# Performance work log

Measured on AMD Instinct MI355X. Metric: run time of the kernel, lower is better.

## Reference

```python
import jax, jax.numpy as jnp
import numpy as np

B = 16384
D = 768           # roberta hidden
SENT = 3          # sentiment features
GRU_IN = D + SENT # 771
H = 128           # memory_dim
FUSION = GRU_IN + H + D  # 1667
E = 7             # num_emotions
S = 65536         # number of (dialog, speaker) memory slots


def setup_inputs() -> dict:
    key = jax.random.key(0)
    ks = jax.random.split(key, 12)
    inp = {
        "h_t": jax.random.normal(ks[0], (B, D), jnp.float32),
        "h_ctx": jax.random.normal(ks[1], (B, D), jnp.float32),
        "sentiment": jax.random.uniform(ks[2], (B, SENT), jnp.float32),
        "slot_ids": jax.random.randint(ks[3], (B,), 0, S, jnp.int32),
        # speaker memory table (gathered/scattered by slot_ids)
        "memory": jax.random.normal(ks[4], (S, H), jnp.float32) * 0.1,
        # GRUCell params (torch layout: rows ordered [r; z; n])
        "W_ih": jax.random.normal(ks[5], (3 * H, GRU_IN), jnp.float32) * 0.02,
        "W_hh": jax.random.normal(ks[6], (3 * H, H), jnp.float32) * 0.02,
        "b_ih": jnp.zeros((3 * H,), jnp.float32),
        "b_hh": jnp.zeros((3 * H,), jnp.float32),
        # heads
        "W_e": jax.random.normal(ks[7], (E, FUSION), jnp.float32) * 0.02,
        "b_e": jnp.zeros((E,), jnp.float32),
        "W_s": jax.random.normal(ks[8], (1, FUSION), jnp.float32) * 0.02,
        "b_s": jnp.zeros((1,), jnp.float32),
    }
    return inp


def _gru_cell(x, h, W_ih, W_hh, b_ih, b_hh):
    # x: [B, GRU_IN], h: [B, H]; torch nn.GRUCell semantics
    gi = x @ W_ih.T + b_ih            # [B, 3H]
    gh = h @ W_hh.T + b_hh            # [B, 3H]
    i_r, i_z, i_n = jnp.split(gi, 3, axis=1)
    h_r, h_z, h_n = jnp.split(gh, 3, axis=1)
    r = jax.nn.sigmoid(i_r + h_r)
    z = jax.nn.sigmoid(i_z + h_z)
    n = jnp.tanh(i_n + r * h_n)
    return (1.0 - z) * n + z * h


def reference(h_t, h_ctx, sentiment, slot_ids, memory, W_ih, W_hh, b_ih, b_hh, W_e, b_e, W_s, b_s):
    h_t_aug = jnp.concatenate([h_t, sentiment], axis=1)      # [B, 771]
    s_t = memory[slot_ids]                                    # gather  [B, H]
    s_new = _gru_cell(h_t_aug, s_t, W_ih, W_hh, b_ih, b_hh)   # [B, H]
    # prediction uses the PRE-update memory s_t (as in the torch loop)
    z_t = jnp.concatenate([h_t_aug, s_t, h_ctx], axis=1)      # [B, 1667] (dropout is identity in eval)
    emotion_logits = z_t @ W_e.T + b_e                        # [B, E]
    shift_logits = (z_t @ W_s.T + b_s)[:, 0]                  # [B]
    # matching the sequential dict updates in the original loop)
    new_memory = memory.at[slot_ids].set(s_new)               # [S, H]
    return emotion_logits, shift_logits, new_memory
```

## Files before the change

kernel.cpp:

```cpp
#include <hip/hip_runtime.h>
#include <hip/hip_bf16.h>

#define B_SZ   16384
#define D_SZ   768
#define H_SZ   128
#define S_SZ   65536
#define E_SZ   7

#define NFR    33
#define NSTEP  53

typedef __attribute__((ext_vector_type(8))) short bf16x8;
typedef __attribute__((ext_vector_type(4))) float f32x4;
typedef __attribute__((ext_vector_type(4))) unsigned int u32x4;

#define LD4(p) (*reinterpret_cast<const float4*>(p))
#define MFMA(d, a, b) d = __builtin_amdgcn_mfma_f32_16x16x32_bf16(a, b, d, 0, 0, 0)

#define GLDS(gp, lp) __builtin_amdgcn_global_load_lds(                              \
        (const __attribute__((address_space(1))) unsigned int*)(gp),                \
        (__attribute__((address_space(3))) unsigned int*)(lp), 16, 0, 0)
#define GLDSN(gp, lp) __builtin_amdgcn_global_load_lds(                             \
        (const __attribute__((address_space(1))) unsigned int*)(gp),                \
        (__attribute__((address_space(3))) unsigned int*)(lp), 16, 0, 2)

#define PIPE_BAR(N) do {                                                            \
        asm volatile("s_waitcnt vmcnt(" #N ")" ::: "memory");                       \
        __builtin_amdgcn_sched_barrier(0);                                          \
        __builtin_amdgcn_s_barrier();                                               \
    } while (0)

static __device__ __forceinline__ ushort f2bf(float v) {
    unsigned u = __float_as_uint(v);
    u = (u + 0x7FFFu + ((u >> 16) & 1u)) >> 16;
    return (ushort)u;
}

static __device__ __forceinline__ unsigned pk2(float x, float y) {
    unsigned a = __float_as_uint(x) + 0x8000u;
    unsigned b = __float_as_uint(y) + 0x8000u;
    return __builtin_amdgcn_perm(b, a, 0x07060302);
}

static __device__ __forceinline__ bf16x8 cvt8(float4 a, float4 b) {
    union { unsigned u[4]; bf16x8 v; } r;
    r.u[0] = pk2(a.x, a.y); r.u[1] = pk2(a.z, a.w);
    r.u[2] = pk2(b.x, b.y); r.u[3] = pk2(b.z, b.w);
    return r.v;
}

static __device__ __forceinline__ float w2_value(int n, int k,
    const float* __restrict__ W_ih, const float* __restrict__ W_hh,
    const float* __restrict__ b_ih, const float* __restrict__ b_hh,
    const float* __restrict__ W_e,  const float* __restrict__ b_e,
    const float* __restrict__ W_s,  const float* __restrict__ b_s)
{
    float v = 0.0f;
    if (n < 256) {
        if (k < 768)                        v = W_ih[(size_t)n * 771 + k];
        else if (k < 896)                   v = W_hh[(size_t)n * 128 + (k - 768)];
        else if (k >= 1664 && k < 1667)     v = W_ih[(size_t)n * 771 + 768 + (k - 1664)];
        else if (k == 1667)                 v = b_ih[n] + b_hh[n];
    } else if (n < 384) {
        if (k < 768)                        v = W_ih[(size_t)n * 771 + k];
        else if (k >= 1664 && k < 1667)     v = W_ih[(size_t)n * 771 + 768 + (k - 1664)];
        else if (k == 1667)                 v = b_ih[n];
    } else if (n < 512) {
        int g = n - 128;
        if (k >= 768 && k < 896)            v = W_hh[(size_t)g * 128 + (k - 768)];
        else if (k == 1667)                 v = b_hh[g];
    } else if (n < 520) {
        int e = n - 512;
        const float* Wr = (e < E_SZ) ? (W_e + (size_t)e * 1667) : W_s;
        if (k < 768)                        v = Wr[k];
        else if (k < 896)                   v = Wr[771 + (k - 768)];
        else if (k < 1664)                  v = Wr[899 + (k - 896)];
        else if (k < 1667)                  v = Wr[768 + (k - 1664)];
        else if (k == 1667)                 v = (e < E_SZ) ? b_e[e] : b_s[0];
    }
    return v;
}

__global__ __launch_bounds__(256) void pack_w2f_kernel(
    const float* __restrict__ W_ih, const float* __restrict__ W_hh,
    const float* __restrict__ b_ih, const float* __restrict__ b_hh,
    const float* __restrict__ W_e,  const float* __restrict__ b_e,
    const float* __restrict__ W_s,  const float* __restrict__ b_s,
    ushort* __restrict__ W2f)
{
    int tid = blockIdx.x * 256 + threadIdx.x;
    if (tid >= NFR * NSTEP * 64) return;
    int lane  = tid & 63;
    int kstep = (tid >> 6) % NSTEP;
    int nf    = tid / (NSTEP * 64);
    int n     = nf * 16 + (lane & 15);
    int kbase = kstep * 32 + (lane >> 4) * 8;
    ushort o[8];
#pragma unroll
    for (int j = 0; j < 8; ++j)
        o[j] = f2bf(w2_value(n, kbase + j, W_ih, W_hh, b_ih, b_hh, W_e, b_e, W_s, b_s));
    *reinterpret_cast<uint4*>(W2f + (size_t)tid * 8) = *reinterpret_cast<const uint4*>(o);
}

__global__ __launch_bounds__(256) void winner_kernel(const int* __restrict__ slot_ids,
                                                     int* __restrict__ winner)
{
    int b = blockIdx.x * 256 + threadIdx.x;
    if (b < B_SZ) atomicMax(&winner[slot_ids[b]], b);
}

static __device__ __forceinline__ bf16x8 ldB(const ushort* __restrict__ W2f, int nf, int ks, int lane) {
    return *reinterpret_cast<const bf16x8*>(W2f + ((size_t)(nf * NSTEP + ks) * 64 + lane) * 8);
}

static __device__ __forceinline__ float4 lds_rd(const char* Ab, int st, int row, int h) {
    return *reinterpret_cast<const float4*>(Ab + st * 4096 + row * 128 + ((h ^ (row & 7)) << 4));
}

__global__ __launch_bounds__(512, 4) void fused_kernel(
    const float* __restrict__ h_t,   const float* __restrict__ h_ctx,
    const float* __restrict__ sent,  const int* __restrict__ slot_ids,
    const float* __restrict__ memory,const ushort* __restrict__ W2f,
    const int* __restrict__ winner,
    float* __restrict__ out_emo, float* __restrict__ out_shift, float* __restrict__ out_mem)
{
    __shared__ alignas(16) char  A_st[3 * 16384];
    __shared__ alignas(16) f32x4 redh[2][8 * 64];

    const int tid  = threadIdx.x;
    const int wave = tid >> 6;
    const int lane = tid & 63;
    const int row0 = blockIdx.x * 32;
    const int cl   = lane & 15, kg = lane >> 4;

    const int fR = wave, fZ = 8 + wave, fI = 16 + wave, fH = 24 + wave;

    const int sst   = wave >> 2;
    const int srb   = wave & 3;
    const int srow  = srb * 8 + (lane >> 3);
    const int scg   = (lane & 7) ^ (srow & 7);
    const int sslot = slot_ids[row0 + srow];

    f32x4 z4 = {0.f, 0.f, 0.f, 0.f};
    f32x4 aR0 = z4, aZ0 = z4, aI0 = z4, aH0 = z4;
    f32x4 aR1 = z4, aZ1 = z4, aI1 = z4, aH1 = z4;
    f32x4 hc0 = z4, hc1 = z4;

#define STAGE(C, BASE) do { _Pragma("unroll")                                             \
    for (int q = 0; q < 2; ++q) {                                                         \
        const int st_ = sst + 2 * q;                                                      \
        const int s_  = 4 * (C) + st_;                                                    \
        char* dst_ = (BASE) + st_ * 4096 + srb * 1024;                                    \
        if (s_ < 24)      GLDSN(h_t + (size_t)(row0 + srow) * D_SZ + s_ * 32 + scg * 4, dst_);          \
        else if (s_ < 28) GLDS(memory + (size_t)sslot * H_SZ + (s_ - 24) * 32 + scg * 4, dst_);         \
        else              GLDSN(h_ctx + (size_t)(row0 + srow) * D_SZ + (s_ - 28) * 32 + scg * 4, dst_); \
    } } while (0)

    STAGE(0, A_st); STAGE(1, A_st + 16384);
    PIPE_BAR(2);

    int bc = 0, sb = 2;

#pragma unroll 1
    for (int c = 0; c < 6; ++c) {
        const char* Ab = A_st + bc * 16384;
#pragma unroll
        for (int st = 0; st < 4; ++st) {
            const int s = c * 4 + st;
            bf16x8 B0 = ldB(W2f, fR, s, lane), B1 = ldB(W2f, fZ, s, lane), B2 = ldB(W2f, fI, s, lane);
            float4 x0 = lds_rd(Ab, st, cl, 2 * kg), x1 = lds_rd(Ab, st, cl, 2 * kg + 1);
            bf16x8 a0 = cvt8(x0, x1);
            MFMA(aR0, a0, B0); MFMA(aZ0, a0, B1); MFMA(aI0, a0, B2);
            float4 y0 = lds_rd(Ab, st, 16 + cl, 2 * kg), y1 = lds_rd(Ab, st, 16 + cl, 2 * kg + 1);
            bf16x8 a1 = cvt8(y0, y1);
            MFMA(aR1, a1, B0); MFMA(aZ1, a1, B1); MFMA(aI1, a1, B2);
            if ((s & 7) == wave) {
                bf16x8 Bh = ldB(W2f, 32, s, lane);
                MFMA(hc0, a0, Bh); MFMA(hc1, a1, Bh);
            }
        }
        STAGE(c + 2, A_st + sb * 16384);
        PIPE_BAR(2);
        bc = (bc == 2) ? 0 : bc + 1;
        sb = (sb == 2) ? 0 : sb + 1;
    }

    {
        const char* Ab = A_st + bc * 16384;
#pragma unroll
        for (int t = 0; t < 4; ++t) {
            const int s = 24 + t;
            bf16x8 B0 = ldB(W2f, fR, s, lane), B1 = ldB(W2f, fZ, s, lane), B2 = ldB(W2f, fH, s, lane);
            float4 x0 = lds_rd(Ab, t, cl, 2 * kg), x1 = lds_rd(Ab, t, cl, 2 * kg + 1);
            bf16x8 a0 = cvt8(x0, x1);
            MFMA(aR0, a0, B0); MFMA(aZ0, a0, B1); MFMA(aH0, a0, B2);
            float4 y0 = lds_rd(Ab, t, 16 + cl, 2 * kg), y1 = lds_rd(Ab, t, 16 + cl, 2 * kg + 1);
            bf16x8 a1 = cvt8(y0, y1);
            MFMA(aR1, a1, B0); MFMA(aZ1, a1, B1); MFMA(aH1, a1, B2);
            if (t == wave) {
                bf16x8 Bh = ldB(W2f, 32, s, lane);
                MFMA(hc0, a0, Bh); MFMA(hc1, a1, Bh);
            }
        }
        STAGE(8, A_st + sb * 16384);
        PIPE_BAR(2);
        bc = (bc == 2) ? 0 : bc + 1;
        sb = (sb == 2) ? 0 : sb + 1;
    }

#pragma unroll 1
    for (int c = 7; c <= 10; ++c) {
        const char* Ab = A_st + bc * 16384;
        if ((c & 1) == (wave >> 2)) {
            const int st = wave & 3;
            const int s  = c * 4 + st;
            bf16x8 Bh = ldB(W2f, 32, s, lane);
            float4 x0 = lds_rd(Ab, st, cl, 2 * kg), x1 = lds_rd(Ab, st, cl, 2 * kg + 1);
            MFMA(hc0, cvt8(x0, x1), Bh);
            float4 y0 = lds_rd(Ab, st, 16 + cl, 2 * kg), y1 = lds_rd(Ab, st, 16 + cl, 2 * kg + 1);
            MFMA(hc1, cvt8(y0, y1), Bh);
        }
        STAGE(c + 2, A_st + sb * 16384);
        PIPE_BAR(2);
        bc = (bc == 2) ? 0 : bc + 1;
        sb = (sb == 2) ? 0 : sb + 1;
    }

    {
        const char* Ab = A_st + bc * 16384;
        if ((wave >> 2) == 1) {
            const int st = wave & 3;
            bf16x8 Bh = ldB(W2f, 32, 44 + st, lane);
            float4 x0 = lds_rd(Ab, st, cl, 2 * kg), x1 = lds_rd(Ab, st, cl, 2 * kg + 1);
            MFMA(hc0, cvt8(x0, x1), Bh);
            float4 y0 = lds_rd(Ab, st, 16 + cl, 2 * kg), y1 = lds_rd(Ab, st, 16 + cl, 2 * kg + 1);
            MFMA(hc1, cvt8(y0, y1), Bh);
        }
        PIPE_BAR(0);
        bc = (bc == 2) ? 0 : bc + 1;
    }

    {
        const char* Ab = A_st + bc * 16384;
        if ((wave >> 2) == 0) {
            const int st = wave & 3;
            bf16x8 Bh = ldB(W2f, 32, 48 + st, lane);
            float4 x0 = lds_rd(Ab, st, cl, 2 * kg), x1 = lds_rd(Ab, st, cl, 2 * kg + 1);
            MFMA(hc0, cvt8(x0, x1), Bh);
            float4 y0 = lds_rd(Ab, st, 16 + cl, 2 * kg), y1 = lds_rd(Ab, st, 16 + cl, 2 * kg + 1);
            MFMA(hc1, cvt8(y0, y1), Bh);
        }
        const int rA0 = row0 + cl, rA1 = rA0 + 16;
        bf16x8 a0, a1;
#pragma unroll
        for (int jj = 0; jj < 8; ++jj) {
            int kk = kg * 8 + jj;
            float v0 = 0.f, v1 = 0.f;
            if (kk < 3)       { v0 = sent[(size_t)rA0 * 3 + kk]; v1 = sent[(size_t)rA1 * 3 + kk]; }
            else if (kk == 3) { v0 = 1.f; v1 = 1.f; }
            a0[jj] = (short)f2bf(v0); a1[jj] = (short)f2bf(v1);
        }
        bf16x8 T0 = ldB(W2f, fR, 52, lane), T1 = ldB(W2f, fZ, 52, lane);
        bf16x8 T2 = ldB(W2f, fI, 52, lane), T3 = ldB(W2f, fH, 52, lane);
        MFMA(aR0, a0, T0); MFMA(aZ0, a0, T1); MFMA(aI0, a0, T2); MFMA(aH0, a0, T3);
        MFMA(aR1, a1, T0); MFMA(aZ1, a1, T1); MFMA(aI1, a1, T2); MFMA(aH1, a1, T3);
        if (wave == 4) {
            bf16x8 Bh = ldB(W2f, 32, 52, lane);
            MFMA(hc0, a0, Bh); MFMA(hc1, a1, Bh);
        }
        const int j = 16 * wave + cl;
#pragma unroll
        for (int rg = 0; rg < 2; ++rg) {
            const f32x4 rv = rg ? aR1 : aR0, zv = rg ? aZ1 : aZ0;
            const f32x4 iv = rg ? aI1 : aI0, hv4 = rg ? aH1 : aH0;
#pragma unroll
            for (int rr = 0; rr < 4; ++rr) {
                const int row  = row0 + rg * 16 + kg * 4 + rr;
                const int slot = slot_ids[row];
                const bool win = (winner[slot] == row);
                float rgate = 1.0f / (1.0f + __expf(-rv[rr]));
                float zg    = 1.0f / (1.0f + __expf(-zv[rr]));
                float nn    = tanhf(iv[rr] + rgate * hv4[rr]);
                float h     = memory[(size_t)slot * H_SZ + j];
                float sn    = (1.0f - zg) * nn + zg * h;
                if (win) out_mem[(size_t)slot * H_SZ + j] = sn;
            }
        }
    }

#pragma unroll 1
    for (int k = 0; k < 8; ++k) {
        int idx  = k * 512 + tid;
        int rr   = idx >> 5;
        int c4   = (idx & 31) * 4;
        int slot = blockIdx.x * 128 + rr;
        if (winner[slot] < 0) {
            u32x4 v = __builtin_nontemporal_load(
                reinterpret_cast<const u32x4*>(memory + (size_t)slot * H_SZ + c4));
            __builtin_nontemporal_store(v,
                reinterpret_cast<u32x4*>(out_mem + (size_t)slot * H_SZ + c4));
        }
    }

    __syncthreads();
    redh[0][wave * 64 + lane] = hc0;
    redh[1][wave * 64 + lane] = hc1;
    __syncthreads();
    if (tid < 128) {
        const int rg = tid >> 6, l = tid & 63;
        f32x4 hv = redh[rg][l];
#pragma unroll
        for (int w = 1; w < 8; ++w) hv += redh[rg][w * 64 + l];
        const int col  = l & 15;
        const int rowb = row0 + rg * 16 + (l >> 4) * 4;
#pragma unroll
        for (int rr = 0; rr < 4; ++rr) {
            const int row = rowb + rr;
            if (col < E_SZ)       out_emo[(size_t)row * E_SZ + col] = hv[rr];
            else if (col == E_SZ) out_shift[row] = hv[rr];
        }
    }
#undef STAGE
}

extern "C" void kernel_launch(void* const* d_in, const int* in_sizes, int n_in,
                              void* d_out, int out_size, void* d_ws, size_t ws_size,
                              hipStream_t stream)
{
    const float* h_t     = (const float*)d_in[0];
    const float* h_ctx   = (const float*)d_in[1];
    const float* sent    = (const float*)d_in[2];
    const int*   slot_ids= (const int*)  d_in[3];
    const float* memory  = (const float*)d_in[4];
    const float* W_ih    = (const float*)d_in[5];
    const float* W_hh    = (const float*)d_in[6];
    const float* b_ih    = (const float*)d_in[7];
    const float* b_hh    = (const float*)d_in[8];
    const float* W_e     = (const float*)d_in[9];
    const float* b_e     = (const float*)d_in[10];
    const float* W_s     = (const float*)d_in[11];
    const float* b_s     = (const float*)d_in[12];

    float* out       = (float*)d_out;
    float* out_emo   = out;
    float* out_shift = out + (size_t)B_SZ * E_SZ;
    float* out_mem   = out + (size_t)B_SZ * E_SZ + B_SZ;

    int*    winner = (int*)d_ws;
    ushort* W2f    = (ushort*)((char*)d_ws + (size_t)S_SZ * sizeof(int));

    hipMemsetAsync(winner, 0xFF, (size_t)S_SZ * sizeof(int), stream);

    pack_w2f_kernel<<<(NFR * NSTEP * 64 + 255) / 256, 256, 0, stream>>>(
        W_ih, W_hh, b_ih, b_hh, W_e, b_e, W_s, b_s, W2f);
    winner_kernel<<<B_SZ / 256, 256, 0, stream>>>(slot_ids, winner);
    fused_kernel<<<B_SZ / 32, 512, 0, stream>>>(
        h_t, h_ctx, sent, slot_ids, memory, W2f, winner, out_emo, out_shift, out_mem);
}
```

Before: 74.46 us.

## Halve LDS staging chunk size and reduction buffer to double occupancy

Shrinks each pipeline stage from four k-steps to two, cutting the triple-buffered LDS staging area from 48KB to 24KB. The head reduction now reuses a single buffer across two passes. Launch bounds go from 4 to 8 blocks per CU so more blocks can be resident to hide gather and load latency. The cost is twice as many pipeline barriers and stage iterations, plus a tighter register budget per thread that may cause spills.

Result: slower. 130.8 us (+75.7%).

```diff
diff --git a/kernel.cpp b/kernel.cpp
--- a/kernel.cpp
+++ b/kernel.cpp
@@ -117,15 +117,15 @@
     return *reinterpret_cast<const float4*>(Ab + st * 4096 + row * 128 + ((h ^ (row & 7)) << 4));
 }
 
-__global__ __launch_bounds__(512, 4) void fused_kernel(
+__global__ __launch_bounds__(512, 8) void fused_kernel(
     const float* __restrict__ h_t,   const float* __restrict__ h_ctx,
     const float* __restrict__ sent,  const int* __restrict__ slot_ids,
     const float* __restrict__ memory,const ushort* __restrict__ W2f,
     const int* __restrict__ winner,
     float* __restrict__ out_emo, float* __restrict__ out_shift, float* __restrict__ out_mem)
 {
-    __shared__ alignas(16) char  A_st[3 * 16384];
-    __shared__ alignas(16) f32x4 redh[2][8 * 64];
+    __shared__ alignas(16) char  A_st[3 * 8192];
+    __shared__ alignas(16) f32x4 redh[8 * 64];
 
     const int tid  = threadIdx.x;
     const int wave = tid >> 6;
@@ -146,27 +146,25 @@
     f32x4 aR1 = z4, aZ1 = z4, aI1 = z4, aH1 = z4;
     f32x4 hc0 = z4, hc1 = z4;
 
-#define STAGE(C, BASE) do { _Pragma("unroll")                                             \
-    for (int q = 0; q < 2; ++q) {                                                         \
-        const int st_ = sst + 2 * q;                                                      \
-        const int s_  = 4 * (C) + st_;                                                    \
-        char* dst_ = (BASE) + st_ * 4096 + srb * 1024;                                    \
+#define STAGE(C, BASE) do {                                                               \
+        const int s_ = 2 * (C) + sst;                                                     \
+        char* dst_ = (BASE) + sst * 4096 + srb * 1024;                                    \
         if (s_ < 24)      GLDSN(h_t + (size_t)(row0 + srow) * D_SZ + s_ * 32 + scg * 4, dst_);          \
         else if (s_ < 28) GLDS(memory + (size_t)sslot * H_SZ + (s_ - 24) * 32 + scg * 4, dst_);         \
         else              GLDSN(h_ctx + (size_t)(row0 + srow) * D_SZ + (s_ - 28) * 32 + scg * 4, dst_); \
-    } } while (0)
-
-    STAGE(0, A_st); STAGE(1, A_st + 16384);
-    PIPE_BAR(2);
+    } while (0)
+
+    STAGE(0, A_st); STAGE(1, A_st + 8192);
+    PIPE_BAR(1);
 
     int bc = 0, sb = 2;
 
 #pragma unroll 1
-    for (int c = 0; c < 6; ++c) {
-        const char* Ab = A_st + bc * 16384;
-#pragma unroll
-        for (int st = 0; st < 4; ++st) {
-            const int s = c * 4 + st;
+    for (int c = 0; c < 12; ++c) {
+        const char* Ab = A_st + bc * 8192;
+#pragma unroll
+        for (int st = 0; st < 2; ++st) {
+            const int s = c * 2 + st;
             bf16x8 B0 = ldB(W2f, fR, s, lane), B1 = ldB(W2f, fZ, s, lane), B2 = ldB(W2f, fI, s, lane);
             float4 x0 = lds_rd(Ab, st, cl, 2 * kg), x1 = lds_rd(Ab, st, cl, 2 * kg + 1);
             bf16x8 a0 = cvt8(x0, x1);
@@ -179,76 +177,85 @@
                 MFMA(hc0, a0, Bh); MFMA(hc1, a1, Bh);
             }
         }
-        STAGE(c + 2, A_st + sb * 16384);
-        PIPE_BAR(2);
+        STAGE(c + 2, A_st + sb * 8192);
+        PIPE_BAR(1);
         bc = (bc == 2) ? 0 : bc + 1;
         sb = (sb == 2) ? 0 : sb + 1;
     }
 
-    {
-        const char* Ab = A_st + bc * 16384;
-#pragma unroll
-        for (int t = 0; t < 4; ++t) {
-            const int s = 24 + t;
+#pragma unroll 1
+    for (int c = 12; c < 14; ++c) {
+        const char* Ab = A_st + bc * 8192;
+#pragma unroll
+        for (int st = 0; st < 2; ++st) {
+            const int s = c * 2 + st;
             bf16x8 B0 = ldB(W2f, fR, s, lane), B1 = ldB(W2f, fZ, s, lane), B2 = ldB(W2f, fH, s, lane);
-            float4 x0 = lds_rd(Ab, t, cl, 2 * kg), x1 = lds_rd(Ab, t, cl, 2 * kg + 1);
+            float4 x0 = lds_rd(Ab, st, cl, 2 * kg), x1 = lds_rd(Ab, st, cl, 2 * kg + 1);
             bf16x8 a0 = cvt8(x0, x1);
             MFMA(aR0, a0, B0); MFMA(aZ0, a0, B1); MFMA(aH0, a0, B2);
-            float4 y0 = lds_rd(Ab, t, 16 + cl, 2 * kg), y1 = lds_rd(Ab, t, 16 + cl, 2 * kg + 1);
+            float4 y0 = lds_rd(Ab, st, 16 + cl, 2 * kg), y1 = lds_rd(Ab, st, 16 + cl, 2 * kg + 1);
             bf16x8 a1 = cvt8(y0, y1);
             MFMA(aR1, a1, B0); MFMA(aZ1, a1, B1); MFMA(aH1, a1, B2);
-            if (t == wave) {
+            if ((s & 7) == wave) {
                 bf16x8 Bh = ldB(W2f, 32, s, lane);
                 MFMA(hc0, a0, Bh); MFMA(hc1, a1, Bh);
             }
         }
-        STAGE(8, A_st + sb * 16384);
-        PIPE_BAR(2);
+        STAGE(c + 2, A_st + sb * 8192);
+        PIPE_BAR(1);
         bc = (bc == 2) ? 0 : bc + 1;
         sb = (sb == 2) ? 0 : sb + 1;
     }
 
 #pragma unroll 1
-    for (int c = 7; c <= 10; ++c) {
-        const char* Ab = A_st + bc * 16384;
-        if ((c & 1) == (wave >> 2)) {
-            const int st = wave & 3;
-            const int s  = c * 4 + st;
-            bf16x8 Bh = ldB(W2f, 32, s, lane);
-            float4 x0 = lds_rd(Ab, st, cl, 2 * kg), x1 = lds_rd(Ab, st, cl, 2 * kg + 1);
-            MFMA(hc0, cvt8(x0, x1), Bh);
-            float4 y0 = lds_rd(Ab, st, 16 + cl, 2 * kg), y1 = lds_rd(Ab, st, 16 + cl, 2 * kg + 1);
-            MFMA(hc1, cvt8(y0, y1), Bh);
-        }
-        STAGE(c + 2, A_st + sb * 16384);
-        PIPE_BAR(2);
+    for (int c = 14; c < 24; ++c) {
+        const char* Ab = A_st + bc * 8192;
+#pragma unroll
+        for (int st = 0; st < 2; ++st) {
+            const int s = c * 2 + st;
+            if ((s & 7) == wave) {
+                bf16x8 Bh = ldB(W2f, 32, s, lane);
+                float4 x0 = lds_rd(Ab, st, cl, 2 * kg), x1 = lds_rd(Ab, st, cl, 2 * kg + 1);
+                MFMA(hc0, cvt8(x0, x1), Bh);
+                float4 y0 = lds_rd(Ab, st, 16 + cl, 2 * kg), y1 = lds_rd(Ab, st, 16 + cl, 2 * kg + 1);
+                MFMA(hc1, cvt8(y0, y1), Bh);
+            }
+        }
+        STAGE(c + 2, A_st + sb * 8192);
+        PIPE_BAR(1);
         bc = (bc == 2) ? 0 : bc + 1;
         sb = (sb == 2) ? 0 : sb + 1;
     }
 
     {
-        const char* Ab = A_st + bc * 16384;
-        if ((wave >> 2) == 1) {
-            const int st = wave & 3;
-            bf16x8 Bh = ldB(W2f, 32, 44 + st, lane);
-            float4 x0 = lds_rd(Ab, st, cl, 2 * kg), x1 = lds_rd(Ab, st, cl, 2 * kg + 1);
-            MFMA(hc0, cvt8(x0, x1), Bh);
-            float4 y0 = lds_rd(Ab, st, 16 + cl, 2 * kg), y1 = lds_rd(Ab, st, 16 + cl, 2 * kg + 1);
-            MFMA(hc1, cvt8(y0, y1), Bh);
+        const char* Ab = A_st + bc * 8192;
+#pragma unroll
+        for (int st = 0; st < 2; ++st) {
+            const int s = 48 + st;
+            if ((s & 7) == wave) {
+                bf16x8 Bh = ldB(W2f, 32, s, lane);
+                float4 x0 = lds_rd(Ab, st, cl, 2 * kg), x1 = lds_rd(Ab, st, cl, 2 * kg + 1);
+                MFMA(hc0, cvt8(x0, x1), Bh);
+                float4 y0 = lds_rd(Ab, st, 16 + cl, 2 * kg), y1 = lds_rd(Ab, st, 16 + cl, 2 * kg + 1);
+                MFMA(hc1, cvt8(y0, y1), Bh);
+            }
         }
         PIPE_BAR(0);
         bc = (bc == 2) ? 0 : bc + 1;
     }
 
     {
-        const char* Ab = A_st + bc * 16384;
-        if ((wave >> 2) == 0) {
-            const int st = wave & 3;
-            bf16x8 Bh = ldB(W2f, 32, 48 + st, lane);
-            float4 x0 = lds_rd(Ab, st, cl, 2 * kg), x1 = lds_rd(Ab, st, cl, 2 * kg + 1);
-            MFMA(hc0, cvt8(x0, x1), Bh);
-            float4 y0 = lds_rd(Ab, st, 16 + cl, 2 * kg), y1 = lds_rd(Ab, st, 16 + cl, 2 * kg + 1);
-            MFMA(hc1, cvt8(y0, y1), Bh);
+        const char* Ab = A_st + bc * 8192;
+#pragma unroll
+        for (int st = 0; st < 2; ++st) {
+            const int s = 50 + st;
+            if ((s & 7) == wave) {
+                bf16x8 Bh = ldB(W2f, 32, s, lane);
+                float4 x0 = lds_rd(Ab, st, cl, 2 * kg), x1 = lds_rd(Ab, st, cl, 2 * kg + 1);
+                MFMA(hc0, cvt8(x0, x1), Bh);
+                float4 y0 = lds_rd(Ab, st, 16 + cl, 2 * kg), y1 = lds_rd(Ab, st, 16 + cl, 2 * kg + 1);
+                MFMA(hc1, cvt8(y0, y1), Bh);
+            }
         }
         const int rA0 = row0 + cl, rA1 = rA0 + 16;
         bf16x8 a0, a1;
@@ -302,22 +309,23 @@
         }
     }
 
-    __syncthreads();
-    redh[0][wave * 64 + lane] = hc0;
-    redh[1][wave * 64 + lane] = hc1;
-    __syncthreads();
-    if (tid < 128) {
-        const int rg = tid >> 6, l = tid & 63;
-        f32x4 hv = redh[rg][l];
-#pragma unroll
-        for (int w = 1; w < 8; ++w) hv += redh[rg][w * 64 + l];
-        const int col  = l & 15;
-        const int rowb = row0 + rg * 16 + (l >> 4) * 4;
-#pragma unroll
-        for (int rr = 0; rr < 4; ++rr) {
-            const int row = rowb + rr;
-            if (col < E_SZ)       out_emo[(size_t)row * E_SZ + col] = hv[rr];
-            else if (col == E_SZ) out_shift[row] = hv[rr];
+#pragma unroll 1
+    for (int rg = 0; rg < 2; ++rg) {
+        __syncthreads();
+        redh[wave * 64 + lane] = rg ? hc1 : hc0;
+        __syncthreads();
+        if (tid < 64) {
+            f32x4 hv = redh[tid];
+#pragma unroll
+            for (int w = 1; w < 8; ++w) hv += redh[w * 64 + tid];
+            const int col  = tid & 15;
+            const int rowb = row0 + rg * 16 + (tid >> 4) * 4;
+#pragma unroll
+            for (int rr = 0; rr < 4; ++rr) {
+                const int row = rowb + rr;
+                if (col < E_SZ)       out_emo[(size_t)row * E_SZ + col] = hv[rr];
+                else if (col == E_SZ) out_shift[row] = hv[rr];
+            }
         }
     }
 #undef STAGE
```
